# Optimization experiments

Hardware: AMD Instinct MI355X
Metric: run time of the kernel (lower is better)

The kernel has to match this reference:

```python
import jax, jax.numpy as jnp
import numpy as np

B, S, D, H, DK, NQ, DFF = 4, 2048, 512, 8, 64, 4, 2048
EPS = 1e-5  # torch LayerNorm default


def setup_inputs() -> dict:
    key = jax.random.key(0)
    ks = jax.random.split(key, 8)
    sc = 1.0 / np.sqrt(D)
    inp = {"x": jax.random.normal(ks[0], (B, S, D), jnp.float32)}
    inp["wq"] = jax.random.normal(ks[1], (D, D), jnp.float32) * sc
    inp["bq"] = jnp.zeros((D,), jnp.float32)
    inp["wk"] = jax.random.normal(ks[2], (D, D), jnp.float32) * sc
    inp["bk"] = jnp.zeros((D,), jnp.float32)
    inp["wv"] = jax.random.normal(ks[3], (D, D), jnp.float32) * sc
    inp["bv"] = jnp.zeros((D,), jnp.float32)
    inp["wo"] = jax.random.normal(ks[4], (D, D), jnp.float32) * sc
    inp["bo"] = jnp.zeros((D,), jnp.float32)
    inp["w1"] = jax.random.normal(ks[5], (D, DFF), jnp.float32) * sc
    inp["b1"] = jnp.zeros((DFF,), jnp.float32)
    inp["w2"] = jax.random.normal(ks[6], (DFF, D), jnp.float32) * (1.0 / np.sqrt(DFF))
    inp["b2"] = jnp.zeros((D,), jnp.float32)
    inp["g1"] = jnp.ones((D,), jnp.float32)
    inp["be1"] = jnp.zeros((D,), jnp.float32)
    inp["g2"] = jnp.ones((D,), jnp.float32)
    inp["be2"] = jnp.zeros((D,), jnp.float32)
    return inp


def _layernorm(x, g, b):
    m = x.mean(-1, keepdims=True)
    v = ((x - m) ** 2).mean(-1, keepdims=True)
    return (x - m) * jax.lax.rsqrt(v + EPS) * g + b


def _forward(x, wq, bq, wk, bk, wv, bv, wo, bo, w1, b1, w2, b2, g1, be1, g2, be2):
    Bx, Sx, Dx = x.shape

    def heads(w, b):  # [B,S,D] -> [B,H,S,DK]
        return (x @ w + b).reshape(Bx, Sx, H, DK).transpose(0, 2, 1, 3)

    q, k, v = heads(wq, bq), heads(wk, bk), heads(wv, bv)
    # Quantum circuit 'execute' yields a uniform distribution over 2^NQ bitstrings,
    # so score = E_s[(qn.s)(kn.s)] = 0.25*(sum(qn)*sum(kn) + qn.kn) over the first
    # NQ components of each head slice (closed form of the original Python loops).
    qn, kn = q[..., :NQ], k[..., :NQ]
    scores = 0.25 * (
        qn.sum(-1)[..., :, None] * kn.sum(-1)[..., None, :]
        + jnp.einsum('bhin,bhjn->bhij', qn, kn)
    )
    attn = jax.nn.softmax(scores, axis=-1)  # [B,H,S,S]
    o = jnp.einsum('bhij,bhjd->bhid', attn, v)
    o = o.transpose(0, 2, 1, 3).reshape(Bx, Sx, Dx) @ wo + bo
    x1 = _layernorm(x + o, g1, be1)  # dropout is identity in eval
    ff = jax.nn.relu(x1 @ w1 + b1) @ w2 + b2
    return _layernorm(x1 + ff, g2, be2)


def reference(x, wq, bq, wk, bk, wv, bv, wo, bo, w1, b1, w2, b2, g1, be1, g2, be2):
    return _forward(x, wq, bq, wk, bk, wv, bv, wo, bo, w1, b1, w2, b2, g1, be1, g2, be2)
```

## Files before the change

kernel.cpp:

```cpp
#include <hip/hip_runtime.h>
#include <cstdint>

#define B_   4
#define S_   2048
#define D_   512
#define H_   8
#define DFF_ 2048

typedef __attribute__((ext_vector_type(4))) float  f32x4;
typedef __attribute__((ext_vector_type(4))) int    i32x4;
typedef __attribute__((ext_vector_type(2))) unsigned int u32x2;
typedef __attribute__((ext_vector_type(4))) unsigned int u32x4;
typedef __attribute__((ext_vector_type(8))) unsigned short u16x8;

#define VMCNT(n)    asm volatile("s_waitcnt vmcnt(" #n ")" ::: "memory")
#define BARRIER_RAW asm volatile("s_barrier" ::: "memory")

__device__ inline void mfma_bf16(f32x4& acc, i32x4 a, i32x4 b) {
  asm("v_mfma_f32_16x16x32_bf16 %0, %1, %2, %0" : "+v"(acc) : "v"(a), "v"(b));
}
__device__ inline unsigned cvt_pk_bf16(float lo, float hi) {
  unsigned r;
  asm("v_cvt_pk_bf16_f32 %0, %1, %2" : "=v"(r) : "v"(lo), "v"(hi));
  return r;
}
__device__ inline unsigned short f2b(float f) {
  unsigned u = __builtin_bit_cast(unsigned, f);
  u += 0x7fffu + ((u >> 16) & 1u);
  return (unsigned short)(u >> 16);
}
__device__ inline float b2f(unsigned short u) {
  return __builtin_bit_cast(float, ((unsigned)u) << 16);
}
__device__ inline void gload_lds16(const void* g, void* l) {
  __builtin_amdgcn_global_load_lds(
      (const __attribute__((address_space(1))) void*)g,
      (__attribute__((address_space(3))) void*)l, 16, 0, 0);
}

__device__ inline void tconv_body(const float* __restrict__ src,
                                  unsigned short* __restrict__ dst,
                                  int RK, int CN, int bx, int by, int tid,
                                  float (*t)[65]) {
  const int tr0 = by * 64, tc0 = bx * 64;
  const int c4 = (tid & 15) * 4, rr = tid >> 4;
#pragma unroll
  for (int i = 0; i < 4; ++i) {
    int r = i * 16 + rr;
    f32x4 v = *(const f32x4*)(src + (size_t)(tr0 + r) * CN + tc0 + c4);
    t[r][c4] = v[0]; t[r][c4 + 1] = v[1]; t[r][c4 + 2] = v[2]; t[r][c4 + 3] = v[3];
  }
  __syncthreads();
#pragma unroll
  for (int i = 0; i < 4; ++i) {
    int oc = i * 16 + rr;
    unsigned lo = cvt_pk_bf16(t[c4][oc], t[c4 + 1][oc]);
    unsigned hi = cvt_pk_bf16(t[c4 + 2][oc], t[c4 + 3][oc]);
    u32x2 pk = {lo, hi};
    *(u32x2*)(dst + (size_t)(tc0 + oc) * RK + tr0 + c4) = pk;
  }
}

__global__ __launch_bounds__(256) void prep_kernel(
    const float* __restrict__ x,
    const float* __restrict__ wq, const float* __restrict__ bq,
    const float* __restrict__ wk, const float* __restrict__ bk,
    const float* __restrict__ wv, const float* __restrict__ bv,
    const float* __restrict__ wo,
    const float* __restrict__ w1, const float* __restrict__ w2,
    unsigned short* __restrict__ xb, unsigned short* __restrict__ wvb,
    unsigned short* __restrict__ wob, unsigned short* __restrict__ w1b,
    unsigned short* __restrict__ w2b, unsigned short* __restrict__ wqkb,
    float* __restrict__ biasv2) {
  __shared__ float tsh[64][65];
  const int blk = blockIdx.x, tid = threadIdx.x;
  if (blk < 2048) {
    size_t i = ((size_t)blk * 256 + tid) * 8;
    f32x4 a = *(const f32x4*)(x + i);
    f32x4 b = *(const f32x4*)(x + i + 4);
    u32x4 o = {cvt_pk_bf16(a[0], a[1]), cvt_pk_bf16(a[2], a[3]),
               cvt_pk_bf16(b[0], b[1]), cvt_pk_bf16(b[2], b[3])};
    *(u32x4*)(xb + i) = o;
  } else if (blk < 2112) {
    int c = blk - 2048;
    const float* w; const float* bb; int scol;
    if (c < 32) { w = wq; bb = bq; scol = (c >> 2) * 64 + (c & 3); }
    else { int c2 = c - 32; w = wk; bb = bk; scol = (c2 >> 2) * 64 + (c2 & 3); }
    for (int k = tid; k < 512; k += 256)
      wqkb[c * 512 + k] = f2b(w[(size_t)k * 512 + scol]);
    if (tid == 0) biasv2[512 + c] = bb[scol];
  } else if (blk < 2176) {
    int lb = blk - 2112;
    tconv_body(wv, wvb, 512, 512, lb & 7, lb >> 3, tid, tsh);
  } else if (blk < 2240) {
    int lb = blk - 2176;
    tconv_body(wo, wob, 512, 512, lb & 7, lb >> 3, tid, tsh);
  } else if (blk < 2496) {
    int lb = blk - 2240;
    tconv_body(w1, w1b, 512, 2048, lb & 31, lb >> 5, tid, tsh);
  } else if (blk < 2752) {
    int lb = blk - 2496;
    tconv_body(w2, w2b, 2048, 512, lb & 7, lb >> 3, tid, tsh);
  } else {
    int i = (blk - 2752) * 256 + tid;
    biasv2[i] = bv[i];
  }
}

template<int WM, int WN, int FM, int FN, int EPI>
__global__ __launch_bounds__(256) void gemm_kernel(
    const unsigned short* __restrict__ A, const unsigned short* __restrict__ Bt,
    const float* __restrict__ bias, void* __restrict__ Cout,
    void* __restrict__ Cout2, int M, int N, int K) {
  constexpr int BM = WM * FM * 16, BN = WN * FN * 16;
  constexpr int ACH = BM * 4, TCH = (BM + BN) * 4;
  constexpr int NS = TCH / 256;
  constexpr int BUFSZ = (BM + BN) * 64;
  __shared__ alignas(16) char lds[3][BUFSZ];
  const int tid = threadIdx.x, lane = tid & 63;
  const int wv = tid >> 6, wr = wv / WN, wc = wv % WN;
  const int bm0 = blockIdx.y * BM, bn0 = blockIdx.x * BN;
  const int l16 = lane & 15, lg = lane >> 4;

  auto stage = [&](int buf, int k0) {
#pragma unroll
    for (int i = 0; i < NS; ++i) {
      int ci = i * 256 + tid;
      const unsigned short* src;
      if (ci < ACH) {
        int r = ci >> 2, gs = ci & 3, g = gs ^ ((r >> 1) & 3);
        src = A + (size_t)(bm0 + r) * K + k0 + g * 8;
      } else {
        int cj = ci - ACH;
        int r = cj >> 2, gs = cj & 3, g = gs ^ ((r >> 1) & 3);
        src = Bt + (size_t)(bn0 + r) * K + k0 + g * 8;
      }
      gload_lds16(src, &lds[buf][ci * 16]);
    }
  };

  f32x4 acc[FM][FN];
#pragma unroll
  for (int i = 0; i < FM; ++i)
#pragma unroll
    for (int j = 0; j < FN; ++j) acc[i][j] = (f32x4){0.f, 0.f, 0.f, 0.f};

  const int T = K >> 5;
  stage(0, 0);
  if (T > 1) stage(1, 32);
  if constexpr (NS == 2) VMCNT(2); else if constexpr (NS == 3) VMCNT(3); else VMCNT(4);
  BARRIER_RAW;

  for (int t = 0; t < T; ++t) {
    const int cur = t % 3;
    const bool more = (t + 2 < T);
    if (more) stage((t + 2) % 3, (t + 2) << 5);

    i32x4 af[FM], bf[FN];
#pragma unroll
    for (int fm = 0; fm < FM; ++fm) {
      int r = wr * FM * 16 + fm * 16 + l16;
      int gs = lg ^ ((r >> 1) & 3);
      af[fm] = *(const i32x4*)(&lds[cur][r * 64 + gs * 16]);
    }
#pragma unroll
    for (int fn = 0; fn < FN; ++fn) {
      int r = wc * FN * 16 + fn * 16 + l16;
      int gs = lg ^ ((r >> 1) & 3);
      bf[fn] = *(const i32x4*)(&lds[cur][BM * 64 + r * 64 + gs * 16]);
    }
    __builtin_amdgcn_s_setprio(1);
#pragma unroll
    for (int fm = 0; fm < FM; ++fm)
#pragma unroll
      for (int fn = 0; fn < FN; ++fn)
        mfma_bf16(acc[fm][fn], af[fm], bf[fn]);
    __builtin_amdgcn_s_setprio(0);

    if (more) {
      if constexpr (NS == 2) VMCNT(2); else if constexpr (NS == 3) VMCNT(3); else VMCNT(4);
    } else {
      VMCNT(0);
    }
    BARRIER_RAW;
  }

#pragma unroll
  for (int fm = 0; fm < FM; ++fm) {
#pragma unroll
    for (int fn = 0; fn < FN; ++fn) {
      f32x4 a = acc[fm][fn];
      int gm = bm0 + wr * FM * 16 + fm * 16 + lg * 4;
      int gn = bn0 + wc * FN * 16 + fn * 16 + l16;
      float bz = bias[gn];
      if constexpr (EPI == 0) {
        float* C = (float*)Cout;
#pragma unroll
        for (int r = 0; r < 4; ++r) C[(size_t)(gm + r) * N + gn] = a[r] + bz;
      } else if constexpr (EPI == 1 || EPI == 2) {
        unsigned short* C = (unsigned short*)Cout;
#pragma unroll
        for (int r = 0; r < 4; ++r) {
          float v = a[r] + bz;
          if constexpr (EPI == 2) v = fmaxf(v, 0.f);
          C[(size_t)(gm + r) * N + gn] = f2b(v);
        }
      } else {
        if (gn < 512) {
          unsigned short* C = (unsigned short*)Cout;
          int b = gm >> 11, s = gm & 2047;
          int h = gn >> 6, d = gn & 63;
          u32x2 pk = {cvt_pk_bf16(a[0] + bz, a[1] + bz),
                      cvt_pk_bf16(a[2] + bz, a[3] + bz)};
          *(u32x2*)(C + (((size_t)(b * 8 + h)) * 64 + d) * 2048 + s) = pk;
        } else {
          float* qtp = (float*)Cout2;
          int c = (gn - 512) & 31, hh = c >> 2, nn = c & 3;
#pragma unroll
          for (int r = 0; r < 4; ++r) {
            float v = a[r] + bz;
            float s4 = v + __shfl_xor(v, 1);
            s4 += __shfl_xor(s4, 2);
            int gmr = gm + r, bb = gmr >> 11, ss = gmr & 2047;
            size_t oi = (((size_t)(bb * 8 + hh)) * 2048 + ss) * 4 + nn;
            if (gn < 544) qtp[oi] = 0.25f * v;
            else          qtp[262144 + oi] = v + s4;
          }
        }
      }
    }
  }
}

__global__ __launch_bounds__(256) void attn_kernel(
    const float* __restrict__ qt, const float* __restrict__ kh,
    const unsigned short* __restrict__ vt, unsigned short* __restrict__ O) {
  __shared__ alignas(16) char vlds[3][8192];
  const int tid = threadIdx.x, lane = tid & 63, wv = tid >> 6;
  const int L = blockIdx.x;
  const int x8 = L & 7, r8 = L >> 3;
  const int bh = x8 + 8 * (r8 & 3), qblk = r8 >> 2;
  const int b = bh >> 3, h = bh & 7;
  const int i0 = qblk * 64;
  const int l16 = lane & 15, g = lane >> 4;
  const int qrow = i0 + wv * 16 + l16;
  const float4 q = *(const float4*)(qt + ((size_t)bh * 2048 + qrow) * 4);
  const float* khb = kh + (size_t)bh * 2048 * 4;
  const unsigned short* vtb = vt + (size_t)bh * 64 * 2048;

  auto stage = [&](int buf, int j0) {
#pragma unroll
    for (int i = 0; i < 2; ++i) {
      int ci = i * 256 + tid;
      int d = ci >> 3, gs = ci & 7, gg = gs ^ (d & 7);
      gload_lds16(vtb + (size_t)d * 2048 + j0 + gg * 8, &vlds[buf][ci * 16]);
    }
  };

  f32x4 acc[4];
#pragma unroll
  for (int i = 0; i < 4; ++i) acc[i] = (f32x4){0.f, 0.f, 0.f, 0.f};
  float lsum = 0.f;

  stage(0, 0);
  stage(1, 64);
  VMCNT(2);
  BARRIER_RAW;

  for (int t = 0; t < 32; ++t) {
    const int cur = t % 3;
    const bool more = (t + 2 < 32);
    if (more) stage((t + 2) % 3, (t + 2) * 64);

    const int j0 = t * 64;
    f32x4 kv[16];
#pragma unroll
    for (int u = 0; u < 16; ++u)
      kv[u] = *(const f32x4*)(khb + (size_t)(j0 + (u >> 3) * 32 + g * 8 + (u & 7)) * 4);

#pragma unroll
    for (int ks = 0; ks < 2; ++ks) {
      float p[8];
#pragma unroll
      for (int jj = 0; jj < 8; ++jj) {
        f32x4 c = kv[ks * 8 + jj];
        float s = q.x * c[0] + q.y * c[1] + q.z * c[2] + q.w * c[3];
        p[jj] = __expf(s);
        lsum += p[jj];
      }
      i32x4 pb = {(int)cvt_pk_bf16(p[0], p[1]), (int)cvt_pk_bf16(p[2], p[3]),
                  (int)cvt_pk_bf16(p[4], p[5]), (int)cvt_pk_bf16(p[6], p[7])};
      __builtin_amdgcn_s_setprio(1);
#pragma unroll
      for (int dt = 0; dt < 4; ++dt) {
        int d = dt * 16 + l16;
        int gg = (ks * 4 + g) ^ (d & 7);
        i32x4 av = *(const i32x4*)(&vlds[cur][d * 128 + gg * 16]);
        mfma_bf16(acc[dt], av, pb);
      }
      __builtin_amdgcn_s_setprio(0);
    }

    if (more) VMCNT(2); else VMCNT(0);
    BARRIER_RAW;
  }

  lsum += __shfl_xor(lsum, 16);
  lsum += __shfl_xor(lsum, 32);
  const float rin = __fdividef(1.f, lsum);
  unsigned short* ob = O + ((size_t)(b * 2048 + qrow)) * 512 + h * 64;
#pragma unroll
  for (int dt = 0; dt < 4; ++dt) {
    f32x4 o = acc[dt] * rin;
    u32x2 pk = {cvt_pk_bf16(o[0], o[1]), cvt_pk_bf16(o[2], o[3])};
    *(u32x2*)(ob + dt * 16 + g * 4) = pk;
  }
}

__global__ __launch_bounds__(256) void ln1_kernel(const float* __restrict__ x,
                                                  const unsigned short* __restrict__ ob,
                                                  const float* __restrict__ g,
                                                  const float* __restrict__ be,
                                                  unsigned short* __restrict__ x1b) {
  const int row = blockIdx.x * 4 + (threadIdx.x >> 6), lane = threadIdx.x & 63;
  const float* xr = x + (size_t)row * 512 + lane * 8;
  f32x4 a0 = *(const f32x4*)xr, a1 = *(const f32x4*)(xr + 4);
  u16x8 rb = *(const u16x8*)(ob + (size_t)row * 512 + lane * 8);
  float v[8];
#pragma unroll
  for (int i = 0; i < 4; ++i) v[i] = a0[i] + b2f(rb[i]);
#pragma unroll
  for (int i = 0; i < 4; ++i) v[4 + i] = a1[i] + b2f(rb[4 + i]);
  float sum = 0.f;
#pragma unroll
  for (int i = 0; i < 8; ++i) sum += v[i];
#pragma unroll
  for (int m = 1; m < 64; m <<= 1) sum += __shfl_xor(sum, m);
  const float mean = sum * (1.f / 512.f);
  float vs = 0.f;
#pragma unroll
  for (int i = 0; i < 8; ++i) { v[i] -= mean; vs += v[i] * v[i]; }
#pragma unroll
  for (int m = 1; m < 64; m <<= 1) vs += __shfl_xor(vs, m);
  const float rs = rsqrtf(vs * (1.f / 512.f) + 1e-5f);
  const f32x4 g0 = *(const f32x4*)(g + lane * 8), g1 = *(const f32x4*)(g + lane * 8 + 4);
  const f32x4 b0 = *(const f32x4*)(be + lane * 8), b1 = *(const f32x4*)(be + lane * 8 + 4);
  float o[8];
#pragma unroll
  for (int i = 0; i < 4; ++i) o[i] = v[i] * rs * g0[i] + b0[i];
#pragma unroll
  for (int i = 0; i < 4; ++i) o[4 + i] = v[4 + i] * rs * g1[i] + b1[i];
  u32x4 pk = {cvt_pk_bf16(o[0], o[1]), cvt_pk_bf16(o[2], o[3]),
              cvt_pk_bf16(o[4], o[5]), cvt_pk_bf16(o[6], o[7])};
  *(u32x4*)(x1b + (size_t)row * 512 + lane * 8) = pk;
}

__global__ __launch_bounds__(256) void ln2_kernel(const unsigned short* __restrict__ x1b,
                                                  float* __restrict__ io,
                                                  const float* __restrict__ g,
                                                  const float* __restrict__ be) {
  const int row = blockIdx.x * 4 + (threadIdx.x >> 6), lane = threadIdx.x & 63;
  float* r = io + (size_t)row * 512 + lane * 8;
  f32x4 a0 = *(const f32x4*)r, a1 = *(const f32x4*)(r + 4);
  u16x8 rb = *(const u16x8*)(x1b + (size_t)row * 512 + lane * 8);
  float v[8];
#pragma unroll
  for (int i = 0; i < 4; ++i) v[i] = a0[i] + b2f(rb[i]);
#pragma unroll
  for (int i = 0; i < 4; ++i) v[4 + i] = a1[i] + b2f(rb[4 + i]);
  float sum = 0.f;
#pragma unroll
  for (int i = 0; i < 8; ++i) sum += v[i];
#pragma unroll
  for (int m = 1; m < 64; m <<= 1) sum += __shfl_xor(sum, m);
  const float mean = sum * (1.f / 512.f);
  float vs = 0.f;
#pragma unroll
  for (int i = 0; i < 8; ++i) { v[i] -= mean; vs += v[i] * v[i]; }
#pragma unroll
  for (int m = 1; m < 64; m <<= 1) vs += __shfl_xor(vs, m);
  const float rs = rsqrtf(vs * (1.f / 512.f) + 1e-5f);
  const f32x4 g0 = *(const f32x4*)(g + lane * 8), g1 = *(const f32x4*)(g + lane * 8 + 4);
  const f32x4 b0 = *(const f32x4*)(be + lane * 8), b1 = *(const f32x4*)(be + lane * 8 + 4);
  f32x4 o0, o1;
#pragma unroll
  for (int i = 0; i < 4; ++i) o0[i] = v[i] * rs * g0[i] + b0[i];
#pragma unroll
  for (int i = 0; i < 4; ++i) o1[i] = v[4 + i] * rs * g1[i] + b1[i];
  *(f32x4*)r = o0;
  *(f32x4*)(r + 4) = o1;
}

extern "C" void kernel_launch(void* const* d_in, const int* in_sizes, int n_in,
                              void* d_out, int out_size, void* d_ws, size_t ws_size,
                              hipStream_t stream) {
  const float* x   = (const float*)d_in[0];
  const float* wq  = (const float*)d_in[1];
  const float* bq  = (const float*)d_in[2];
  const float* wk  = (const float*)d_in[3];
  const float* bk  = (const float*)d_in[4];
  const float* wv  = (const float*)d_in[5];
  const float* bv  = (const float*)d_in[6];
  const float* wo  = (const float*)d_in[7];
  const float* bo  = (const float*)d_in[8];
  const float* w1  = (const float*)d_in[9];
  const float* b1  = (const float*)d_in[10];
  const float* w2  = (const float*)d_in[11];
  const float* b2  = (const float*)d_in[12];
  const float* g1  = (const float*)d_in[13];
  const float* be1 = (const float*)d_in[14];
  const float* g2  = (const float*)d_in[15];
  const float* be2 = (const float*)d_in[16];
  float* out = (float*)d_out;
  char* ws = (char*)d_ws;

  unsigned short* wvb    = (unsigned short*)(ws + 0x000000);
  unsigned short* wqkb   = (unsigned short*)(ws + 0x080000);
  float*          biasv2 = (float*)         (ws + 0x090000);
  unsigned short* wob    = (unsigned short*)(ws + 0x0A0000);
  unsigned short* w1b    = (unsigned short*)(ws + 0x120000);
  unsigned short* w2b    = (unsigned short*)(ws + 0x320000);
  float*          qt     = (float*)         (ws + 0x520000);
  float*          kh     = (float*)         (ws + 0x620000);
  unsigned short* x1b    = (unsigned short*)(ws + 0x720000);
  unsigned short* xb     = (unsigned short*)(ws + 0xF20000);
  unsigned short* Ob     = (unsigned short*)(ws + 0xF20000);
  unsigned short* hidden = (unsigned short*)(ws + 0xF20000);
  unsigned short* vtb    = (unsigned short*)(ws + 0x1720000);
  unsigned short* oprojb = (unsigned short*)(ws + 0x1720000);

  prep_kernel<<<2754, 256, 0, stream>>>(x, wq, bq, wk, bk, wv, bv, wo, w1, w2,
                                        xb, wvb, wob, w1b, w2b, wqkb, biasv2);

  gemm_kernel<2, 2, 4, 2, 5><<<dim3(9, 64), 256, 0, stream>>>(
      xb, wvb, biasv2, vtb, qt, 8192, 576, 512);

  attn_kernel<<<1024, 256, 0, stream>>>(qt, kh, vtb, Ob);

  gemm_kernel<2, 2, 4, 2, 1><<<dim3(8, 64), 256, 0, stream>>>(
      Ob, wob, bo, oprojb, nullptr, 8192, 512, 512);

  ln1_kernel<<<2048, 256, 0, stream>>>(x, oprojb, g1, be1, x1b);

  for (int c = 0; c < 2; ++c) {
    const unsigned short* x1c = x1b + (size_t)c * 4096 * 512;
    float* outc = out + (size_t)c * 4096 * 512;
    gemm_kernel<2, 2, 4, 4, 2><<<dim3(16, 32), 256, 0, stream>>>(
        x1c, w1b, b1, hidden, nullptr, 4096, 2048, 512);
    gemm_kernel<2, 2, 4, 2, 0><<<dim3(8, 32), 256, 0, stream>>>(
        hidden, w2b, b2, outc, nullptr, 4096, 512, 2048);
  }

  ln2_kernel<<<2048, 256, 0, stream>>>(x1b, out, g2, be2);
}
```

Measured before the change: 212.4 us.

## Store key projections as fp16 and stage whole head's keys into LDS

The QKV GEMM epilogue now writes the folded key vectors as fp16 instead of fp32, halving that buffer, and the workspace layout is shifted to match. The attention kernel loads all 2048 keys of its head into a 16 KB LDS buffer once at the start, using global_load_lds, instead of issuing per-tile global vector loads. Score computation then reads packed fp16 pairs from LDS. This cuts global key traffic and per-iteration load latency, at the cost of fp16 precision on keys and extra LDS use that may lower occupancy.

```diff
diff --git a/kernel.cpp b/kernel.cpp
--- a/kernel.cpp
+++ b/kernel.cpp
@@ -12,6 +12,7 @@
 typedef __attribute__((ext_vector_type(2))) unsigned int u32x2;
 typedef __attribute__((ext_vector_type(4))) unsigned int u32x4;
 typedef __attribute__((ext_vector_type(8))) unsigned short u16x8;
+typedef __attribute__((ext_vector_type(8))) _Float16 f16x8;
 
 #define VMCNT(n)    asm volatile("s_waitcnt vmcnt(" #n ")" ::: "memory")
 #define BARRIER_RAW asm volatile("s_barrier" ::: "memory")
@@ -31,6 +32,10 @@
 }
 __device__ inline float b2f(unsigned short u) {
   return __builtin_bit_cast(float, ((unsigned)u) << 16);
+}
+__device__ inline unsigned short f2h(float f) {
+  _Float16 h = (_Float16)f;
+  return __builtin_bit_cast(unsigned short, h);
 }
 __device__ inline void gload_lds16(const void* g, void* l) {
   __builtin_amdgcn_global_load_lds(
@@ -215,6 +220,7 @@
           *(u32x2*)(C + (((size_t)(b * 8 + h)) * 64 + d) * 2048 + s) = pk;
         } else {
           float* qtp = (float*)Cout2;
+          unsigned short* kh16 = (unsigned short*)(qtp + 262144);
           int c = (gn - 512) & 31, hh = c >> 2, nn = c & 3;
 #pragma unroll
           for (int r = 0; r < 4; ++r) {
@@ -224,7 +230,7 @@
             int gmr = gm + r, bb = gmr >> 11, ss = gmr & 2047;
             size_t oi = (((size_t)(bb * 8 + hh)) * 2048 + ss) * 4 + nn;
             if (gn < 544) qtp[oi] = 0.25f * v;
-            else          qtp[262144 + oi] = v + s4;
+            else          kh16[oi] = f2h(v + s4);
           }
         }
       }
@@ -233,9 +239,10 @@
 }
 
 __global__ __launch_bounds__(256) void attn_kernel(
-    const float* __restrict__ qt, const float* __restrict__ kh,
+    const float* __restrict__ qt, const unsigned short* __restrict__ kh16,
     const unsigned short* __restrict__ vt, unsigned short* __restrict__ O) {
   __shared__ alignas(16) char vlds[3][8192];
+  __shared__ alignas(16) char khl[16384];
   const int tid = threadIdx.x, lane = tid & 63, wv = tid >> 6;
   const int L = blockIdx.x;
   const int x8 = L & 7, r8 = L >> 3;
@@ -245,7 +252,7 @@
   const int l16 = lane & 15, g = lane >> 4;
   const int qrow = i0 + wv * 16 + l16;
   const float4 q = *(const float4*)(qt + ((size_t)bh * 2048 + qrow) * 4);
-  const float* khb = kh + (size_t)bh * 2048 * 4;
+  const char* khb = (const char*)(kh16 + (size_t)bh * 2048 * 4);
   const unsigned short* vtb = vt + (size_t)bh * 64 * 2048;
 
   auto stage = [&](int buf, int j0) {
@@ -262,6 +269,11 @@
   for (int i = 0; i < 4; ++i) acc[i] = (f32x4){0.f, 0.f, 0.f, 0.f};
   float lsum = 0.f;
 
+#pragma unroll
+  for (int i = 0; i < 4; ++i) {
+    int ci = i * 256 + tid;
+    gload_lds16(khb + ci * 16, khl + ci * 16);
+  }
   stage(0, 0);
   stage(1, 64);
   VMCNT(2);
@@ -271,22 +283,21 @@
     const int cur = t % 3;
     const bool more = (t + 2 < 32);
     if (more) stage((t + 2) % 3, (t + 2) * 64);
-
     const int j0 = t * 64;
-    f32x4 kv[16];
-#pragma unroll
-    for (int u = 0; u < 16; ++u)
-      kv[u] = *(const f32x4*)(khb + (size_t)(j0 + (u >> 3) * 32 + g * 8 + (u & 7)) * 4);
 
 #pragma unroll
     for (int ks = 0; ks < 2; ++ks) {
       float p[8];
 #pragma unroll
-      for (int jj = 0; jj < 8; ++jj) {
-        f32x4 c = kv[ks * 8 + jj];
-        float s = q.x * c[0] + q.y * c[1] + q.z * c[2] + q.w * c[3];
-        p[jj] = __expf(s);
-        lsum += p[jj];
+      for (int u = 0; u < 4; ++u) {
+        f16x8 kk = *(const f16x8*)(khl + (size_t)(j0 + ks * 32 + g * 8 + u * 2) * 8);
+        float s0 = q.x * (float)kk[0] + q.y * (float)kk[1] +
+                   q.z * (float)kk[2] + q.w * (float)kk[3];
+        float s1 = q.x * (float)kk[4] + q.y * (float)kk[5] +
+                   q.z * (float)kk[6] + q.w * (float)kk[7];
+        p[u * 2]     = __expf(s0);
+        p[u * 2 + 1] = __expf(s1);
+        lsum += p[u * 2] + p[u * 2 + 1];
       }
       i32x4 pb = {(int)cvt_pk_bf16(p[0], p[1]), (int)cvt_pk_bf16(p[2], p[3]),
                   (int)cvt_pk_bf16(p[4], p[5]), (int)cvt_pk_bf16(p[6], p[7])};
@@ -421,13 +432,13 @@
   unsigned short* w1b    = (unsigned short*)(ws + 0x120000);
   unsigned short* w2b    = (unsigned short*)(ws + 0x320000);
   float*          qt     = (float*)         (ws + 0x520000);
-  float*          kh     = (float*)         (ws + 0x620000);
-  unsigned short* x1b    = (unsigned short*)(ws + 0x720000);
-  unsigned short* xb     = (unsigned short*)(ws + 0xF20000);
-  unsigned short* Ob     = (unsigned short*)(ws + 0xF20000);
-  unsigned short* hidden = (unsigned short*)(ws + 0xF20000);
-  unsigned short* vtb    = (unsigned short*)(ws + 0x1720000);
-  unsigned short* oprojb = (unsigned short*)(ws + 0x1720000);
+  unsigned short* kh16   = (unsigned short*)(ws + 0x620000);
+  unsigned short* x1b    = (unsigned short*)(ws + 0x6A0000);
+  unsigned short* xb     = (unsigned short*)(ws + 0xEA0000);
+  unsigned short* Ob     = (unsigned short*)(ws + 0xEA0000);
+  unsigned short* hidden = (unsigned short*)(ws + 0xEA0000);
+  unsigned short* vtb    = (unsigned short*)(ws + 0x16A0000);
+  unsigned short* oprojb = (unsigned short*)(ws + 0x16A0000);
 
   prep_kernel<<<2754, 256, 0, stream>>>(x, wq, bq, wk, bk, wv, bv, wo, w1, w2,
                                         xb, wvb, wob, w1b, w2b, wqkb, biasv2);
@@ -435,7 +446,7 @@
   gemm_kernel<2, 2, 4, 2, 5><<<dim3(9, 64), 256, 0, stream>>>(
       xb, wvb, biasv2, vtb, qt, 8192, 576, 512);
 
-  attn_kernel<<<1024, 256, 0, stream>>>(qt, kh, vtb, Ob);
+  attn_kernel<<<1024, 256, 0, stream>>>(qt, kh16, vtb, Ob);
 
   gemm_kernel<2, 2, 4, 2, 1><<<dim3(8, 64), 256, 0, stream>>>(
       Ob, wob, bo, oprojb, nullptr, 8192, 512, 512);
```

New measurement: 200.3 us (median of 3 runs). -5.7%, faster.
